# Kernel tuning notes

Hardware: AMD Instinct MI355X
Metric: run time of the kernel (lower is better)

Reference implementation:

```python
import jax, jax.numpy as jnp
import numpy as np

D = 1024           # fusion_dim
H_MHA = 16         # fusion_heads
H_GAT = 8          # graph attention heads
GAT_DH = D // H_GAT
DIL = (1, 2, 4, 8, 16)
K = 7              # temporal_kernel_size
B, T = 8, 256


def setup_inputs() -> dict:
    key = jax.random.key(0)
    ks = jax.random.split(key, 20)

    def w(k, sh, fan):
        return jax.random.normal(k, sh, jnp.float32) * np.float32(1.0 / np.sqrt(fan))

    inp = {"features": jax.random.normal(ks[0], (B, T, D), jnp.float32)}
    for i, dil in enumerate(DIL):
        inp["conv_w%d" % i] = w(ks[1 + i], (D, D, K), D * K)   # torch Conv1d (out, in, k)
        inp["conv_b%d" % i] = jnp.zeros((D,), jnp.float32)
    inp["fp_w"] = w(ks[6], (D, 5 * D), 5 * D)                    # torch Linear (out, in)
    inp["fp_b"] = jnp.zeros((D,), jnp.float32)
    inp["ln_g"] = jnp.ones((D,), jnp.float32)
    inp["ln_b"] = jnp.zeros((D,), jnp.float32)
    inp["wq"] = w(ks[7], (D, D), D); inp["bq"] = jnp.zeros((D,), jnp.float32)
    inp["wk"] = w(ks[8], (D, D), D); inp["bk"] = jnp.zeros((D,), jnp.float32)
    inp["wv"] = w(ks[9], (D, D), D); inp["bv"] = jnp.zeros((D,), jnp.float32)
    inp["wo"] = w(ks[10], (D, D), D); inp["bo"] = jnp.zeros((D,), jnp.float32)
    inp["gat_w"] = w(ks[11], (D, D), D)
    inp["gat_b"] = jnp.zeros((D,), jnp.float32)
    # original `a` is (2*head_dim, 1) shared across heads; split into a1 (source) / a2 (target)
    inp["gat_a1"] = w(ks[12], (GAT_DH,), 2 * GAT_DH)
    inp["gat_a2"] = w(ks[13], (GAT_DH,), 2 * GAT_DH)
    return inp


def _forward(features, conv_ws, conv_bs, fp_w, fp_b, ln_g, ln_b,
             wq, bq, wk, bk, wv, bv, wo, bo, gat_w, gat_b, gat_a1, gat_a2):
    Bb, Tt, Dm = features.shape
    x = jnp.transpose(features, (0, 2, 1))                       # (B, D, T)
    feats = []
    for wgt, bias, dil in zip(conv_ws, conv_bs, DIL):
        pad = (K - 1) * dil // 2                                 # 'same' padding
        y = jax.lax.conv_general_dilated(
            x, wgt, window_strides=(1,), padding=[(pad, pad)],
            rhs_dilation=(dil,), dimension_numbers=("NCH", "OIH", "NCH"))
        feats.append(jnp.transpose(y + bias[None, :, None], (0, 2, 1)))
    ms = jnp.concatenate(feats, axis=-1)                         # (B, T, 5D)
    z = ms @ fp_w.T + fp_b                                       # (B, T, D)
    mu = jnp.mean(z, -1, keepdims=True)
    var = jnp.var(z, -1, keepdims=True)
    z = (z - mu) * jax.lax.rsqrt(var + 1e-5) * ln_g + ln_b       # LayerNorm
    z = jax.nn.gelu(z, approximate=False)
    # --- multi-head self attention (batch_first, no dropout at eval) ---
    dh = Dm // H_MHA
    q = (z @ wq.T + bq).reshape(Bb, Tt, H_MHA, dh)
    k = (z @ wk.T + bk).reshape(Bb, Tt, H_MHA, dh)
    v = (z @ wv.T + bv).reshape(Bb, Tt, H_MHA, dh)
    scores = jnp.einsum("bqhd,bkhd->bhqk", q, k) * np.float32(1.0 / np.sqrt(dh))
    attn = jax.nn.softmax(scores, axis=-1)
    ctx = jnp.einsum("bhqk,bkhd->bqhd", attn, v).reshape(Bb, Tt, Dm)
    att_out = ctx @ wo.T + bo
    # --- all-pairs graph attention over N = B*T nodes (GAT-style, a shared across heads) ---
    n = Bb * Tt
    hg = (att_out.reshape(n, Dm) @ gat_w.T + gat_b).reshape(n, H_GAT, GAT_DH)
    e1 = jnp.einsum("nhd,d->nh", hg, gat_a1)                     # a1 . h_i
    e2 = jnp.einsum("nhd,d->nh", hg, gat_a2)                     # a2 . h_j
    e = jax.nn.leaky_relu(e1[:, None, :] + e2[None, :, :], 0.2)  # (N, N, H) via broadcast
    alpha = jax.nn.softmax(e, axis=1)                            # normalize over j
    hp = jnp.einsum("ijh,jhd->ihd", alpha, hg).reshape(n, Dm)
    g = jax.nn.elu(hp).reshape(Bb, Tt, Dm)
    return g + features


def reference(features, conv_w0, conv_w1, conv_w2, conv_w3, conv_w4,
              conv_b0, conv_b1, conv_b2, conv_b3, conv_b4,
              fp_w, fp_b, ln_g, ln_b,
              wq, bq, wk, bk, wv, bv, wo, bo,
              gat_w, gat_b, gat_a1, gat_a2):
    return _forward(features,
                    (conv_w0, conv_w1, conv_w2, conv_w3, conv_w4),
                    (conv_b0, conv_b1, conv_b2, conv_b3, conv_b4),
                    fp_w, fp_b, ln_g, ln_b,
                    wq, bq, wk, bk, wv, bv, wo, bo,
                    gat_w, gat_b, gat_a1, gat_a2)
```

## Files before the change

### kernel.cpp

```cpp
#include <hip/hip_runtime.h>
#include <hip/hip_bf16.h>

typedef __bf16 bf16_t;
typedef bf16_t bf16x8 __attribute__((ext_vector_type(8)));
typedef bf16_t bf16x4v __attribute__((ext_vector_type(4)));
typedef float f32x4 __attribute__((ext_vector_type(4)));

__device__ __forceinline__ void gll16(const bf16_t* g, bf16_t* l) {
    __builtin_amdgcn_global_load_lds(
        (const __attribute__((address_space(1))) unsigned int*)g,
        (__attribute__((address_space(3))) unsigned int*)l, 16, 0, 0);
}

__global__ __launch_bounds__(256)
void cvt_f32_bf16(const float* __restrict__ in, bf16_t* __restrict__ out, int n4)
{
    int i = blockIdx.x * 256 + threadIdx.x;
    if (i < n4) {
        float4 v = ((const float4*)in)[i];
        bf16x4v o = { (bf16_t)v.x, (bf16_t)v.y, (bf16_t)v.z, (bf16_t)v.w };
        *(bf16x4v*)&out[i * 4] = o;
    }
}

__global__ __launch_bounds__(256)
void cvt_multi(const float* __restrict__ fpw, const float* __restrict__ wq,
               const float* __restrict__ wk, const float* __restrict__ wv,
               const float* __restrict__ gw,
               bf16_t* __restrict__ fpwb, bf16_t* __restrict__ wqb,
               bf16_t* __restrict__ wkb, bf16_t* __restrict__ wvb,
               bf16_t* __restrict__ gwb)
{
    int id = blockIdx.x * 256 + threadIdx.x;
    const float* src; bf16_t* dst; int off;
    if (id < 1310720) { src = fpw; dst = fpwb; off = id; }
    else {
        int id3 = id - 1310720;
        int w = id3 >> 18; off = id3 & 262143;
        const float* ss[4] = {wq, wk, wv, gw};
        bf16_t* dd[4] = {wqb, wkb, wvb, gwb};
        src = ss[w]; dst = dd[w];
    }
    float4 v = ((const float4*)src)[off];
    bf16x4v o = { (bf16_t)v.x, (bf16_t)v.y, (bf16_t)v.z, (bf16_t)v.w };
    *(bf16x4v*)&dst[off * 4] = o;
}

__global__ __launch_bounds__(256)
void reorder_convw(const float* w0, const float* w1, const float* w2,
                   const float* w3, const float* w4, bf16_t* __restrict__ out)
{
    int gid = blockIdx.x * 256 + threadIdx.x;
    int i = gid >> 20, rem = gid & 1048575;
    int o = rem >> 10, c = rem & 1023;
    const float* ws[5] = {w0, w1, w2, w3, w4};
    const float* src = ws[i] + (size_t)o * 7168 + c * 7;
    #pragma unroll
    for (int kk = 0; kk < 7; kk++)
        out[((size_t)(i * 7 + kk) << 20) + (o << 10) + c] = (bf16_t)src[kk];
}

__global__ __launch_bounds__(256)
void gather_bias(const float* b0, const float* b1, const float* b2,
                 const float* b3, const float* b4,
                 const float* bq, const float* bk,
                 float* __restrict__ out, float* __restrict__ qkbias,
                 bf16_t* __restrict__ zp)
{
    int idx = blockIdx.x * 256 + threadIdx.x;
    if (blockIdx.x == 0 && threadIdx.x < 32) zp[threadIdx.x] = (bf16_t)0.0f;
    if (idx < 5120) {
        const float* bs[5] = {b0, b1, b2, b3, b4};
        out[idx] = bs[idx >> 10][idx & 1023];
    } else {
        int j = idx - 5120;
        qkbias[j] = (j < 1024) ? bq[j] : bk[j - 1024];
    }
}

__global__ __launch_bounds__(256)
void transpose_w(const float* __restrict__ in, bf16_t* __restrict__ out)
{
    __shared__ float tile[32][33];
    const int t = threadIdx.x;
    const int j0 = blockIdx.x * 32, c0 = blockIdx.y * 32;
    {
        int jl = t >> 3, cl = (t & 7) * 4;
        float4 v = *(const float4*)(in + (size_t)(j0 + jl) * 1024 + c0 + cl);
        tile[jl][cl] = v.x; tile[jl][cl + 1] = v.y;
        tile[jl][cl + 2] = v.z; tile[jl][cl + 3] = v.w;
    }
    __syncthreads();
    {
        int cl = t >> 3, jl = (t & 7) * 4;
        bf16x4v o = { (bf16_t)tile[jl][cl], (bf16_t)tile[jl + 1][cl],
                      (bf16_t)tile[jl + 2][cl], (bf16_t)tile[jl + 3][cl] };
        *(bf16x4v*)&out[(size_t)(c0 + cl) * 1024 + j0 + jl] = o;
    }
}

__global__ __launch_bounds__(256)
void fold_bias(const float* __restrict__ gw, const float* __restrict__ bo,
               const float* __restrict__ gb, float* __restrict__ bc)
{
    const int wave = threadIdx.x >> 6, lane = threadIdx.x & 63;
    const int d = blockIdx.x * 4 + wave;
    const float* row = gw + (size_t)d * 1024;
    float s = 0.f;
    #pragma unroll
    for (int k = lane * 4; k < 1024; k += 256) {
        float4 x = *(const float4*)&row[k];
        float4 a = *(const float4*)&bo[k];
        s += x.x * a.x + x.y * a.y + x.z * a.z + x.w * a.w;
    }
    s += __shfl_xor(s, 1);  s += __shfl_xor(s, 2);  s += __shfl_xor(s, 4);
    s += __shfl_xor(s, 8);  s += __shfl_xor(s, 16); s += __shfl_xor(s, 32);
    if (lane == 0) bc[d] = gb[d] + s;
}

template<bool CONV, bool OUT_BF16, bool BIAS_ROW = false, int NR = 128>
__global__ __launch_bounds__(256)
void mfma_gemm(const bf16_t* __restrict__ A, const bf16_t* __restrict__ Bw,
               const float* __restrict__ bias, void* __restrict__ outv,
               const bf16_t* __restrict__ zp,
               int Kd, int lda, int ldb, int ldo, int out_col0)
{
    constexpr int FN = NR / 32;
    __shared__ __align__(16) bf16_t As[3][NR * 32];
    __shared__ __align__(16) bf16_t Bs[3][128 * 32];
    const int t = threadIdx.x;
    const int lane = t & 63, wave = t >> 6;
    const int wn = (wave & 1) * (NR / 2), wm = (wave >> 1) * 64;
    const int q = lane >> 4, lr = lane & 15;
    const int mt = CONV ? (blockIdx.x & 7) : blockIdx.x;
    const int conv_i = CONV ? (blockIdx.x >> 3) : 0;
    const int m0 = mt * 128, n0 = blockIdx.y * NR;
    const int srow = lane >> 2, sseg = lane & 3;
    const int sw_seg = sseg ^ ((srow >> 1) & 3);
    const int slotq = (q ^ ((lr >> 1) & 3)) * 8;

    f32x4 acc[FN][4];
    #pragma unroll
    for (int a = 0; a < FN; a++)
        #pragma unroll
        for (int b = 0; b < 4; b++) acc[a][b] = (f32x4){0.f, 0.f, 0.f, 0.f};

    const int ksteps = Kd >> 5;
    const int T = CONV ? ksteps * 7 : ksteps;

    int s_tap = 0, s_k0 = 0;
    auto do_stage = [&](int bi) {
        const bf16_t* Bp = CONV ? (Bw + ((size_t)(conv_i * 7 + s_tap) << 20)) : Bw;
        const int shift = CONV ? ((s_tap - 3) << conv_i) : 0;
        #pragma unroll
        for (int p = 0; p < NR / 64; p++) {
            const int slab = p * 64 + wave * 16;
            const bf16_t* ga;
            if (CONV) {
                const int slabN = n0 + slab;
                const int inSeg = slabN & 255;
                if (inSeg + shift >= 0 && inSeg + shift <= 240) {
                    ga = A + (size_t)(slabN + srow + shift) * lda + s_k0 + sw_seg * 8;
                } else {
                    int n = slabN + srow;
                    int tg = (n & 255) + shift;
                    ga = ((unsigned)tg < 256u)
                       ? A + (size_t)((n & ~255) + tg) * lda + s_k0 + sw_seg * 8
                       : zp + sseg * 8;
                }
            } else {
                ga = A + (size_t)(n0 + slab + srow) * lda + s_k0 + sw_seg * 8;
            }
            gll16(ga, &As[bi][slab * 32]);
        }
        #pragma unroll
        for (int p = 0; p < 2; p++) {
            const int slab = p * 64 + wave * 16;
            const int rr = slab + srow;
            gll16(Bp + (size_t)(m0 + rr) * ldb + s_k0 + sw_seg * 8, &Bs[bi][slab * 32]);
        }
        s_k0 += 32;
        if (CONV && s_k0 == Kd) { s_k0 = 0; s_tap++; }
    };

    do_stage(0);
    do_stage(1);

    int cur = 0;
    for (int s = 0; s < T; s++) {
        if (s + 1 < T) {
            if constexpr (NR == 128) asm volatile("s_waitcnt vmcnt(4)" ::: "memory");
            else                     asm volatile("s_waitcnt vmcnt(3)" ::: "memory");
        } else {
            asm volatile("s_waitcnt vmcnt(0)" ::: "memory");
        }
        __builtin_amdgcn_s_barrier();
        __builtin_amdgcn_sched_barrier(0);

        bf16x8 af[FN], bfv[4];
        #pragma unroll
        for (int f = 0; f < FN; f++)
            af[f] = *(bf16x8*)&As[cur][(wn + f * 16 + lr) * 32 + slotq];
        #pragma unroll
        for (int f = 0; f < 4; f++)
            bfv[f] = *(bf16x8*)&Bs[cur][(wm + f * 16 + lr) * 32 + slotq];

        int nb = cur + 2; if (nb >= 3) nb -= 3;
        if (s + 2 < T) do_stage(nb);

        __builtin_amdgcn_s_setprio(1);
        #pragma unroll
        for (int fn = 0; fn < FN; fn++)
            #pragma unroll
            for (int fm = 0; fm < 4; fm++)
                acc[fn][fm] = __builtin_amdgcn_mfma_f32_16x16x32_bf16(
                    af[fn], bfv[fm], acc[fn][fm], 0, 0, 0);
        __builtin_amdgcn_s_setprio(0);
        cur++; if (cur == 3) cur = 0;
    }

    const int oc0 = CONV ? (conv_i << 10) : out_col0;
    #pragma unroll
    for (int fn = 0; fn < FN; fn++) {
        #pragma unroll
        for (int r = 0; r < 4; r++) {
            int n = n0 + wn + fn * 16 + q * 4 + r;
            #pragma unroll
            for (int fm = 0; fm < 4; fm++) {
                int m = m0 + wm + fm * 16 + lr;
                float v = acc[fn][fm][r];
                if (bias) v += bias[BIAS_ROW ? n : (oc0 + m)];
                if (OUT_BF16)
                    ((bf16_t*)outv)[(size_t)n * ldo + oc0 + m] = (bf16_t)v;
                else
                    ((float*)outv)[(size_t)n * ldo + oc0 + m] = v;
            }
        }
    }
}

__global__ __launch_bounds__(256)
void ln_gelu(float* __restrict__ z, bf16_t* __restrict__ zb,
             const float* __restrict__ g, const float* __restrict__ b)
{
    __shared__ float r1[256], r2[256];
    const int n = blockIdx.x, t = threadIdx.x;
    float* row = z + (size_t)n * 1024;
    float x[4], s = 0.f, s2 = 0.f;
    #pragma unroll
    for (int u = 0; u < 4; u++) {
        x[u] = row[t + u * 256];
        s += x[u]; s2 += x[u] * x[u];
    }
    r1[t] = s; r2[t] = s2;
    __syncthreads();
    for (int off = 128; off > 0; off >>= 1) {
        if (t < off) { r1[t] += r1[t + off]; r2[t] += r2[t + off]; }
        __syncthreads();
    }
    const float mu  = r1[0] * (1.0f / 1024.0f);
    const float var = r2[0] * (1.0f / 1024.0f) - mu * mu;
    const float rstd = rsqrtf(var + 1e-5f);
    #pragma unroll
    for (int u = 0; u < 4; u++) {
        int c = t + u * 256;
        float y = (x[u] - mu) * rstd * g[c] + b[c];
        float gv = 0.5f * y * (1.0f + erff(y * 0.70710678118654752f));
        row[c] = gv;
        zb[(size_t)n * 1024 + c] = (bf16_t)gv;
    }
}

__global__ __launch_bounds__(256)
void attn_mfma(const bf16_t* __restrict__ qg, const bf16_t* __restrict__ kg,
               const bf16_t* __restrict__ vt, bf16_t* __restrict__ ctx)
{
    const int it = blockIdx.x, h = blockIdx.y, bb = blockIdx.z;
    const int t = threadIdx.x, lane = t & 63, wave = t >> 6;
    const int q4 = lane >> 4, lr = lane & 15;
    const size_t qkbase = (size_t)bb * 256 * 2048 + (size_t)h * 64;

    __shared__ __align__(16) bf16_t Qs[4][32 * 64];
    __shared__ __align__(16) bf16_t Ks[64 * 64];
    __shared__ __align__(16) bf16_t Vs[64 * 64];
    __shared__ __align__(16) bf16_t Ps[4][32 * 64];

    {
        const int itbase = it * 128;
        #pragma unroll
        for (int rep = 0; rep < 4; rep++) {
            int idx = rep * 256 + t;
            int rl = idx >> 3, seg = idx & 7;
            bf16x8 v = *(const bf16x8*)&qg[qkbase + (size_t)(itbase + rl) * 2048 + seg * 8];
            *(bf16x8*)&Qs[rl >> 5][(rl & 31) * 64 + ((seg ^ (rl & 7)) << 3)] = v;
        }
    }

    f32x4 o[2][4];
    float mrow[2][4], lrow[2][4];
    #pragma unroll
    for (int fn = 0; fn < 2; fn++)
        #pragma unroll
        for (int x = 0; x < 4; x++) {
            o[fn][x] = (f32x4){0.f, 0.f, 0.f, 0.f};
            mrow[fn][x] = -1e30f; lrow[fn][x] = 0.f;
        }

    for (int j0 = 0; j0 < 256; j0 += 64) {
        __syncthreads();
        #pragma unroll
        for (int rep = 0; rep < 2; rep++) {
            int idx = rep * 256 + t;
            int rl = idx >> 3, seg = idx & 7;
            bf16x8 kv = *(const bf16x8*)&kg[qkbase + (size_t)(j0 + rl) * 2048 + seg * 8];
            *(bf16x8*)&Ks[rl * 64 + ((seg ^ (rl & 7)) << 3)] = kv;
            bf16x8 vv = *(const bf16x8*)&vt[(size_t)(h * 64 + rl) * 2048 + bb * 256 + j0 + seg * 8];
            *(bf16x8*)&Vs[rl * 64 + ((seg ^ (rl & 7)) << 3)] = vv;
        }
        __syncthreads();

        f32x4 s[2][4];
        #pragma unroll
        for (int fn = 0; fn < 2; fn++)
            #pragma unroll
            for (int fm = 0; fm < 4; fm++) s[fn][fm] = (f32x4){0.f, 0.f, 0.f, 0.f};
        #pragma unroll
        for (int kk = 0; kk < 2; kk++) {
            bf16x8 aq[2], bk[4];
            #pragma unroll
            for (int fn = 0; fn < 2; fn++) {
                int row = fn * 16 + lr;
                aq[fn] = *(bf16x8*)&Qs[wave][row * 64 + (((kk * 4 + q4) ^ (row & 7)) << 3)];
            }
            #pragma unroll
            for (int fm = 0; fm < 4; fm++) {
                int row = fm * 16 + lr;
                bk[fm] = *(bf16x8*)&Ks[row * 64 + (((kk * 4 + q4) ^ (row & 7)) << 3)];
            }
            #pragma unroll
            for (int fn = 0; fn < 2; fn++)
                #pragma unroll
                for (int fm = 0; fm < 4; fm++)
                    s[fn][fm] = __builtin_amdgcn_mfma_f32_16x16x32_bf16(
                        aq[fn], bk[fm], s[fn][fm], 0, 0, 0);
        }

        #pragma unroll
        for (int fn = 0; fn < 2; fn++) {
            #pragma unroll
            for (int r = 0; r < 4; r++) {
                float sv[4];
                #pragma unroll
                for (int fm = 0; fm < 4; fm++) sv[fm] = s[fn][fm][r] * 0.125f;
                float rm = fmaxf(fmaxf(sv[0], sv[1]), fmaxf(sv[2], sv[3]));
                rm = fmaxf(rm, __shfl_xor(rm, 1));
                rm = fmaxf(rm, __shfl_xor(rm, 2));
                rm = fmaxf(rm, __shfl_xor(rm, 4));
                rm = fmaxf(rm, __shfl_xor(rm, 8));
                float mold = mrow[fn][r];
                float mnew = fmaxf(mold, rm);
                float scl = __expf(mold - mnew);
                mrow[fn][r] = mnew;
                int prow = fn * 16 + q4 * 4 + r;
                float psum = 0.f;
                #pragma unroll
                for (int fm = 0; fm < 4; fm++) {
                    float p = __expf(sv[fm] - mnew);
                    psum += p;
                    int col = fm * 16 + lr;
                    Ps[wave][prow * 64 + (col ^ ((prow & 7) << 3))] = (bf16_t)p;
                }
                psum += __shfl_xor(psum, 1);
                psum += __shfl_xor(psum, 2);
                psum += __shfl_xor(psum, 4);
                psum += __shfl_xor(psum, 8);
                lrow[fn][r] = lrow[fn][r] * scl + psum;
                #pragma unroll
                for (int fd = 0; fd < 4; fd++) o[fn][fd][r] *= scl;
            }
        }

        #pragma unroll
        for (int kk = 0; kk < 2; kk++) {
            bf16x8 ap[2], bvf[4];
            #pragma unroll
            for (int fn = 0; fn < 2; fn++) {
                int row = fn * 16 + lr;
                ap[fn] = *(bf16x8*)&Ps[wave][row * 64 + (((kk * 4 + q4) ^ (row & 7)) << 3)];
            }
            #pragma unroll
            for (int fd = 0; fd < 4; fd++) {
                int row = fd * 16 + lr;
                bvf[fd] = *(bf16x8*)&Vs[row * 64 + (((kk * 4 + q4) ^ (row & 7)) << 3)];
            }
            #pragma unroll
            for (int fn = 0; fn < 2; fn++)
                #pragma unroll
                for (int fd = 0; fd < 4; fd++)
                    o[fn][fd] = __builtin_amdgcn_mfma_f32_16x16x32_bf16(
                        ap[fn], bvf[fd], o[fn][fd], 0, 0, 0);
        }
    }

    const int i0 = it * 128 + wave * 32;
    #pragma unroll
    for (int fn = 0; fn < 2; fn++) {
        #pragma unroll
        for (int r = 0; r < 4; r++) {
            float inv = 1.0f / lrow[fn][r];
            int row = i0 + fn * 16 + q4 * 4 + r;
            #pragma unroll
            for (int fd = 0; fd < 4; fd++) {
                int col = h * 64 + fd * 16 + lr;
                ctx[(size_t)bb * 262144 + (size_t)row * 1024 + col] =
                    (bf16_t)(o[fn][fd][r] * inv);
            }
        }
    }
}

__global__ __launch_bounds__(256)
void gat_e(const bf16_t* __restrict__ hgT, const float* __restrict__ a1,
           const float* __restrict__ a2, float* __restrict__ e1t,
           float* __restrict__ e2t)
{
    int id = blockIdx.x * 256 + threadIdx.x;
    int h = id >> 11, n = id & 2047;
    const bf16_t* base = hgT + (size_t)(h * 128) * 2048 + n;
    float s1 = 0.f, s2 = 0.f;
    #pragma unroll 4
    for (int d = 0; d < 128; d++) {
        float x = (float)base[(size_t)d * 2048];
        s1 += x * a1[d];
        s2 += x * a2[d];
    }
    e1t[id] = s1; e2t[id] = s2;
}

__global__ __launch_bounds__(256)
void gat_agg_mfma(const bf16_t* __restrict__ hgT, const float* __restrict__ e1t,
                  const float* __restrict__ e2t, const float* __restrict__ feat,
                  float* __restrict__ outp)
{
    const int it = blockIdx.x, h = blockIdx.y;
    const int i0 = it * 64;
    __shared__ float e2s[2048];
    __shared__ float e1s[64], mS[64], lSinv[64];
    __shared__ float wmax[4];
    __shared__ __align__(16) bf16_t Ps[64 * 136];
    __shared__ __align__(16) bf16_t Hs[128 * 136];
    const int t = threadIdx.x;
    const int lane = t & 63, wave = t >> 6;
    const int q = lane >> 4, lr = lane & 15;
    const int wm = wave * 32;

    float lmax = -1e30f;
    for (int idx = t; idx < 2048; idx += 256) {
        float v = e2t[h * 2048 + idx];
        e2s[idx] = v;
        lmax = fmaxf(lmax, v);
    }
    if (t < 64) e1s[t] = e1t[h * 2048 + i0 + t];
    #pragma unroll
    for (int d = 1; d < 64; d <<= 1) lmax = fmaxf(lmax, __shfl_xor(lmax, d));
    if (lane == 0) wmax[wave] = lmax;
    __syncthreads();
    {
        float maxE2 = fmaxf(fmaxf(wmax[0], wmax[1]), fmaxf(wmax[2], wmax[3]));
        if (t < 64) {
            float x = e1s[t] + maxE2;
            mS[t] = (x >= 0.f) ? x : 0.2f * x;
        }
    }
    __syncthreads();

    f32x4 acc[4][2];
    #pragma unroll
    for (int a = 0; a < 4; a++)
        #pragma unroll
        for (int b = 0; b < 2; b++) acc[a][b] = (f32x4){0.f, 0.f, 0.f, 0.f};
    float psum[4] = {0.f, 0.f, 0.f, 0.f};

    for (int j0 = 0; j0 < 2048; j0 += 128) {
        for (int idx = t; idx < 2048; idx += 256) {
            int d = idx >> 4, seg = idx & 15;
            *(bf16x8*)&Hs[d * 136 + seg * 8] =
                *(const bf16x8*)&hgT[(size_t)(h * 128 + d) * 2048 + j0 + seg * 8];
        }
        #pragma unroll
        for (int rep = 0; rep < 4; rep++) {
            int idx = rep * 256 + t;
            int i = idx >> 4, jg = idx & 15;
            float ei = e1s[i], mi = mS[i];
            bf16x8 pv;
            #pragma unroll
            for (int u = 0; u < 8; u++) {
                float x = ei + e2s[j0 + jg * 8 + u];
                x = (x >= 0.f) ? x : 0.2f * x;
                float p = __expf(x - mi);
                psum[rep] += p;
                pv[u] = (bf16_t)p;
            }
            *(bf16x8*)&Ps[i * 136 + jg * 8] = pv;
        }
        __syncthreads();
        #pragma unroll
        for (int kb = 0; kb < 4; kb++) {
            bf16x8 af[4], bf2[2];
            #pragma unroll
            for (int fn = 0; fn < 4; fn++)
                af[fn] = *(bf16x8*)&Ps[(fn * 16 + lr) * 136 + kb * 32 + q * 8];
            #pragma unroll
            for (int fm = 0; fm < 2; fm++)
                bf2[fm] = *(bf16x8*)&Hs[(wm + fm * 16 + lr) * 136 + kb * 32 + q * 8];
            #pragma unroll
            for (int fn = 0; fn < 4; fn++)
                #pragma unroll
                for (int fm = 0; fm < 2; fm++)
                    acc[fn][fm] = __builtin_amdgcn_mfma_f32_16x16x32_bf16(
                        af[fn], bf2[fm], acc[fn][fm], 0, 0, 0);
        }
        __syncthreads();
    }

    #pragma unroll
    for (int rep = 0; rep < 4; rep++) {
        float v = psum[rep];
        v += __shfl_xor(v, 1);
        v += __shfl_xor(v, 2);
        v += __shfl_xor(v, 4);
        v += __shfl_xor(v, 8);
        if ((t & 15) == 0) lSinv[rep * 16 + (t >> 4)] = 1.0f / v;
    }
    __syncthreads();

    #pragma unroll
    for (int fn = 0; fn < 4; fn++) {
        #pragma unroll
        for (int r = 0; r < 4; r++) {
            int il = fn * 16 + q * 4 + r;
            int i = i0 + il;
            float inv = lSinv[il];
            #pragma unroll
            for (int fm = 0; fm < 2; fm++) {
                int col = h * 128 + wm + fm * 16 + lr;
                float v = acc[fn][fm][r] * inv;
                v = (v > 0.f) ? v : (expf(v) - 1.0f);
                size_t off = (size_t)i * 1024 + col;
                outp[off] = v + feat[off];
            }
        }
    }
}

extern "C" void kernel_launch(void* const* d_in, const int* in_sizes, int n_in,
                              void* d_out, int out_size, void* d_ws, size_t ws_size,
                              hipStream_t stream)
{
    const float* feat = (const float*)d_in[0];
    const float *cw[5], *cb[5];
    if (in_sizes[2] == 1024) {
        for (int i = 0; i < 5; i++) { cw[i] = (const float*)d_in[1 + 2*i]; cb[i] = (const float*)d_in[2 + 2*i]; }
    } else {
        for (int i = 0; i < 5; i++) { cw[i] = (const float*)d_in[1 + i];   cb[i] = (const float*)d_in[6 + i]; }
    }
    const float* fp_w = (const float*)d_in[11];
    const float* fp_b = (const float*)d_in[12];
    const float* ln_g = (const float*)d_in[13];
    const float* ln_b = (const float*)d_in[14];
    const float* wq = (const float*)d_in[15]; const float* bq = (const float*)d_in[16];
    const float* wk = (const float*)d_in[17]; const float* bk = (const float*)d_in[18];
    const float* wv = (const float*)d_in[19]; const float* bv = (const float*)d_in[20];
    const float* wo = (const float*)d_in[21]; const float* bo = (const float*)d_in[22];
    const float* gat_w = (const float*)d_in[23]; const float* gat_b = (const float*)d_in[24];
    const float* ga1 = (const float*)d_in[25]; const float* ga2 = (const float*)d_in[26];
    float* outp = (float*)d_out;

    char* wsb = (char*)d_ws;
    bf16_t* xb    = (bf16_t*)(wsb);
    bf16_t* msb   = (bf16_t*)(wsb + 4194304);
    bf16_t* wcb   = (bf16_t*)(wsb + 25165824);
    float*  zf    = (float*) (wsb + 98566144);
    bf16_t* zb    = (bf16_t*)(wsb + 106954752);
    bf16_t* qb    = (bf16_t*)(wsb + 111149056);
    bf16_t* kb    = (bf16_t*)(wsb + 115343360);
    bf16_t* vb    = (bf16_t*)(wsb + 119537664);
    float*  cball = (float*) (wsb + 123731968);
    float*  e1t   = (float*) (wsb + 123752448);
    float*  e2t   = (float*) (wsb + 123817984);
    bf16_t* zpage = (bf16_t*)(wsb + 123883520);
    bf16_t* fpwb = wcb;
    bf16_t* wqb  = wcb + 5242880;
    bf16_t* wkb  = wqb + 1048576;
    bf16_t* wvb  = wkb + 1048576;
    bf16_t* woTb = wvb + 1048576;
    bf16_t* gwb  = woTb + 1048576;
    bf16_t* qkb  = qb;
    float*  qkbias = e1t;
    bf16_t* ctxb = zb;
    bf16_t* wcomb = xb;
    float*  bcomb = cball;
    bf16_t* hgtb = msb;

    const dim3 blk(256);

    cvt_f32_bf16<<<dim3(2048), blk, 0, stream>>>(feat, xb, 524288);
    reorder_convw<<<dim3(20480), blk, 0, stream>>>(cw[0], cw[1], cw[2], cw[3], cw[4], wcb);
    gather_bias<<<dim3(28), blk, 0, stream>>>(cb[0], cb[1], cb[2], cb[3], cb[4],
                                              bq, bk, cball, qkbias, zpage);

    mfma_gemm<true, true><<<dim3(40, 16), blk, 0, stream>>>(
        xb, wcb, cball, msb, zpage, 1024, 1024, 1024, 5120, 0);

    cvt_multi<<<dim3(9216), blk, 0, stream>>>(fp_w, wq, wk, wv, gat_w,
                                              fpwb, wqb, wkb, wvb, gwb);
    transpose_w<<<dim3(32, 32), blk, 0, stream>>>(wo, woTb);
    fold_bias<<<dim3(256), blk, 0, stream>>>(gat_w, bo, gat_b, bcomb);

    mfma_gemm<false, true, false, 64><<<dim3(8, 16), blk, 0, stream>>>(
        gwb, woTb, nullptr, wcomb, zpage, 1024, 1024, 1024, 1024, 0);

    mfma_gemm<false, false, false, 64><<<dim3(8, 32), blk, 0, stream>>>(
        msb, fpwb, fp_b, zf, zpage, 5120, 5120, 5120, 1024, 0);

    ln_gelu<<<dim3(2048), blk, 0, stream>>>(zf, zb, ln_g, ln_b);

    mfma_gemm<false, true, false, 64><<<dim3(16, 32), blk, 0, stream>>>(
        zb, wqb, qkbias, qkb, zpage, 1024, 1024, 1024, 2048, 0);
    mfma_gemm<false, true, true, 64><<<dim3(16, 16), blk, 0, stream>>>(
        wvb, zb, bv, vb, zpage, 1024, 1024, 1024, 2048, 0);

    attn_mfma<<<dim3(2, 16, 8), blk, 0, stream>>>(qkb, qkb + 1024, vb, ctxb);

    mfma_gemm<false, true, true, 64><<<dim3(16, 16), blk, 0, stream>>>(
        wcomb, ctxb, bcomb, hgtb, zpage, 1024, 1024, 1024, 2048, 0);

    gat_e<<<dim3(64), blk, 0, stream>>>(hgtb, ga1, ga2, e1t, e2t);
    gat_agg_mfma<<<dim3(32, 8), blk, 0, stream>>>(hgtb, e1t, e2t, feat, outp);
}
```

Measured before the change: 658.6 us.

## Merge prep kernels, batch independent GEMMs into dual launches, specialize conv GEMM

The small weight-conversion, bias-gather and transpose kernels are folded into two multi-role prep kernels. The conv weight reorder now stages each output row through shared memory so reads and writes are coalesced. Independent GEMMs (fp projection with the wo/gat weight fold, and QK with V) now share one grid split by blockIdx.y, which cuts launch count and fills more CUs. The conv GEMM becomes a dedicated kernel that precomputes per-tap pointers and steps them incrementally instead of recomputing addresses each k-step, at the cost of more code and extra register pressure.

Measured after the change: 641.1 us. -2.7%, faster.

```diff
diff --git a/kernel.cpp b/kernel.cpp
--- a/kernel.cpp
+++ b/kernel.cpp
@@ -13,128 +13,125 @@
 }
 
 __global__ __launch_bounds__(256)
-void cvt_f32_bf16(const float* __restrict__ in, bf16_t* __restrict__ out, int n4)
-{
-    int i = blockIdx.x * 256 + threadIdx.x;
-    if (i < n4) {
-        float4 v = ((const float4*)in)[i];
+void prep1(const float* w0, const float* w1, const float* w2, const float* w3,
+           const float* w4, const float* feat,
+           const float* b0, const float* b1, const float* b2, const float* b3,
+           const float* b4, const float* bq, const float* bk,
+           bf16_t* __restrict__ wout, bf16_t* __restrict__ xb,
+           float* __restrict__ cball, float* __restrict__ qkbias,
+           bf16_t* __restrict__ zp)
+{
+    __shared__ __align__(16) float s[7168];
+    const int bid = blockIdx.x, t = threadIdx.x;
+    if (bid < 5120) {
+        int i = bid >> 10, o = bid & 1023;
+        const float* ws[5] = {w0, w1, w2, w3, w4};
+        const float* src = ws[i] + (size_t)o * 7168;
+        #pragma unroll
+        for (int r = 0; r < 7; r++)
+            ((float4*)s)[r * 256 + t] = ((const float4*)src)[r * 256 + t];
+        __syncthreads();
+        const int c4 = t * 4;
+        #pragma unroll
+        for (int kk = 0; kk < 7; kk++) {
+            bf16x4v v = { (bf16_t)s[c4 * 7 + kk], (bf16_t)s[(c4 + 1) * 7 + kk],
+                          (bf16_t)s[(c4 + 2) * 7 + kk], (bf16_t)s[(c4 + 3) * 7 + kk] };
+            *(bf16x4v*)&wout[((size_t)(i * 7 + kk) << 20) + (o << 10) + c4] = v;
+        }
+    } else if (bid < 7168) {
+        int i = (bid - 5120) * 256 + t;
+        float4 v = ((const float4*)feat)[i];
+        bf16x4v o4 = { (bf16_t)v.x, (bf16_t)v.y, (bf16_t)v.z, (bf16_t)v.w };
+        *(bf16x4v*)&xb[i * 4] = o4;
+    } else {
+        int idx = (bid - 7168) * 256 + t;
+        if (bid == 7168 && t < 32) zp[t] = (bf16_t)0.0f;
+        if (idx < 5120) {
+            const float* bs[5] = {b0, b1, b2, b3, b4};
+            cball[idx] = bs[idx >> 10][idx & 1023];
+        } else {
+            int j = idx - 5120;
+            qkbias[j] = (j < 1024) ? bq[j] : bk[j - 1024];
+        }
+    }
+}
+
+__global__ __launch_bounds__(256)
+void prep2(const float* __restrict__ fpw, const float* __restrict__ wq,
+           const float* __restrict__ wk, const float* __restrict__ wv,
+           const float* __restrict__ gw, const float* __restrict__ wo,
+           const float* __restrict__ bo, const float* __restrict__ gb,
+           bf16_t* __restrict__ fpwb, bf16_t* __restrict__ wqb,
+           bf16_t* __restrict__ wkb, bf16_t* __restrict__ wvb,
+           bf16_t* __restrict__ gwb, bf16_t* __restrict__ woTb,
+           float* __restrict__ bc)
+{
+    __shared__ float tile[32][33];
+    const int bid = blockIdx.x, t = threadIdx.x;
+    if (bid < 9216) {
+        int id = bid * 256 + t;
+        const float* src; bf16_t* dst; int off;
+        if (id < 1310720) { src = fpw; dst = fpwb; off = id; }
+        else {
+            int id3 = id - 1310720;
+            int w = id3 >> 18; off = id3 & 262143;
+            const float* ss[4] = {wq, wk, wv, gw};
+            bf16_t* dd[4] = {wqb, wkb, wvb, gwb};
+            src = ss[w]; dst = dd[w];
+        }
+        float4 v = ((const float4*)src)[off];
         bf16x4v o = { (bf16_t)v.x, (bf16_t)v.y, (bf16_t)v.z, (bf16_t)v.w };
-        *(bf16x4v*)&out[i * 4] = o;
-    }
-}
-
-__global__ __launch_bounds__(256)
-void cvt_multi(const float* __restrict__ fpw, const float* __restrict__ wq,
-               const float* __restrict__ wk, const float* __restrict__ wv,
-               const float* __restrict__ gw,
-               bf16_t* __restrict__ fpwb, bf16_t* __restrict__ wqb,
-               bf16_t* __restrict__ wkb, bf16_t* __restrict__ wvb,
-               bf16_t* __restrict__ gwb)
-{
-    int id = blockIdx.x * 256 + threadIdx.x;
-    const float* src; bf16_t* dst; int off;
-    if (id < 1310720) { src = fpw; dst = fpwb; off = id; }
-    else {
-        int id3 = id - 1310720;
-        int w = id3 >> 18; off = id3 & 262143;
-        const float* ss[4] = {wq, wk, wv, gw};
-        bf16_t* dd[4] = {wqb, wkb, wvb, gwb};
-        src = ss[w]; dst = dd[w];
-    }
-    float4 v = ((const float4*)src)[off];
-    bf16x4v o = { (bf16_t)v.x, (bf16_t)v.y, (bf16_t)v.z, (bf16_t)v.w };
-    *(bf16x4v*)&dst[off * 4] = o;
-}
-
-__global__ __launch_bounds__(256)
-void reorder_convw(const float* w0, const float* w1, const float* w2,
-                   const float* w3, const float* w4, bf16_t* __restrict__ out)
-{
-    int gid = blockIdx.x * 256 + threadIdx.x;
-    int i = gid >> 20, rem = gid & 1048575;
-    int o = rem >> 10, c = rem & 1023;
-    const float* ws[5] = {w0, w1, w2, w3, w4};
-    const float* src = ws[i] + (size_t)o * 7168 + c * 7;
-    #pragma unroll
-    for (int kk = 0; kk < 7; kk++)
-        out[((size_t)(i * 7 + kk) << 20) + (o << 10) + c] = (bf16_t)src[kk];
-}
-
-__global__ __launch_bounds__(256)
-void gather_bias(const float* b0, const float* b1, const float* b2,
-                 const float* b3, const float* b4,
-                 const float* bq, const float* bk,
-                 float* __restrict__ out, float* __restrict__ qkbias,
-                 bf16_t* __restrict__ zp)
-{
-    int idx = blockIdx.x * 256 + threadIdx.x;
-    if (blockIdx.x == 0 && threadIdx.x < 32) zp[threadIdx.x] = (bf16_t)0.0f;
-    if (idx < 5120) {
-        const float* bs[5] = {b0, b1, b2, b3, b4};
-        out[idx] = bs[idx >> 10][idx & 1023];
+        *(bf16x4v*)&dst[off * 4] = o;
+    } else if (bid < 10240) {
+        int idx = bid - 9216;
+        int j0 = (idx & 31) * 32, c0 = (idx >> 5) * 32;
+        {
+            int jl = t >> 3, cl = (t & 7) * 4;
+            float4 v = *(const float4*)(wo + (size_t)(j0 + jl) * 1024 + c0 + cl);
+            tile[jl][cl] = v.x; tile[jl][cl + 1] = v.y;
+            tile[jl][cl + 2] = v.z; tile[jl][cl + 3] = v.w;
+        }
+        __syncthreads();
+        {
+            int cl = t >> 3, jl = (t & 7) * 4;
+            bf16x4v o = { (bf16_t)tile[jl][cl], (bf16_t)tile[jl + 1][cl],
+                          (bf16_t)tile[jl + 2][cl], (bf16_t)tile[jl + 3][cl] };
+            *(bf16x4v*)&woTb[(size_t)(c0 + cl) * 1024 + j0 + jl] = o;
+        }
     } else {
-        int j = idx - 5120;
-        qkbias[j] = (j < 1024) ? bq[j] : bk[j - 1024];
-    }
-}
-
-__global__ __launch_bounds__(256)
-void transpose_w(const float* __restrict__ in, bf16_t* __restrict__ out)
-{
-    __shared__ float tile[32][33];
-    const int t = threadIdx.x;
-    const int j0 = blockIdx.x * 32, c0 = blockIdx.y * 32;
-    {
-        int jl = t >> 3, cl = (t & 7) * 4;
-        float4 v = *(const float4*)(in + (size_t)(j0 + jl) * 1024 + c0 + cl);
-        tile[jl][cl] = v.x; tile[jl][cl + 1] = v.y;
-        tile[jl][cl + 2] = v.z; tile[jl][cl + 3] = v.w;
-    }
-    __syncthreads();
-    {
-        int cl = t >> 3, jl = (t & 7) * 4;
-        bf16x4v o = { (bf16_t)tile[jl][cl], (bf16_t)tile[jl + 1][cl],
-                      (bf16_t)tile[jl + 2][cl], (bf16_t)tile[jl + 3][cl] };
-        *(bf16x4v*)&out[(size_t)(c0 + cl) * 1024 + j0 + jl] = o;
-    }
-}
-
-__global__ __launch_bounds__(256)
-void fold_bias(const float* __restrict__ gw, const float* __restrict__ bo,
-               const float* __restrict__ gb, float* __restrict__ bc)
-{
-    const int wave = threadIdx.x >> 6, lane = threadIdx.x & 63;
-    const int d = blockIdx.x * 4 + wave;
-    const float* row = gw + (size_t)d * 1024;
-    float s = 0.f;
-    #pragma unroll
-    for (int k = lane * 4; k < 1024; k += 256) {
-        float4 x = *(const float4*)&row[k];
-        float4 a = *(const float4*)&bo[k];
-        s += x.x * a.x + x.y * a.y + x.z * a.z + x.w * a.w;
-    }
-    s += __shfl_xor(s, 1);  s += __shfl_xor(s, 2);  s += __shfl_xor(s, 4);
-    s += __shfl_xor(s, 8);  s += __shfl_xor(s, 16); s += __shfl_xor(s, 32);
-    if (lane == 0) bc[d] = gb[d] + s;
-}
-
-template<bool CONV, bool OUT_BF16, bool BIAS_ROW = false, int NR = 128>
-__global__ __launch_bounds__(256)
-void mfma_gemm(const bf16_t* __restrict__ A, const bf16_t* __restrict__ Bw,
-               const float* __restrict__ bias, void* __restrict__ outv,
-               const bf16_t* __restrict__ zp,
-               int Kd, int lda, int ldb, int ldo, int out_col0)
-{
-    constexpr int FN = NR / 32;
-    __shared__ __align__(16) bf16_t As[3][NR * 32];
-    __shared__ __align__(16) bf16_t Bs[3][128 * 32];
-    const int t = threadIdx.x;
-    const int lane = t & 63, wave = t >> 6;
+        int wave = t >> 6, lane = t & 63;
+        int d = (bid - 10240) * 4 + wave;
+        const float* row = gw + (size_t)d * 1024;
+        float ssum = 0.f;
+        #pragma unroll
+        for (int k = lane * 4; k < 1024; k += 256) {
+            float4 x = *(const float4*)&row[k];
+            float4 a = *(const float4*)&bo[k];
+            ssum += x.x * a.x + x.y * a.y + x.z * a.z + x.w * a.w;
+        }
+        ssum += __shfl_xor(ssum, 1);  ssum += __shfl_xor(ssum, 2);
+        ssum += __shfl_xor(ssum, 4);  ssum += __shfl_xor(ssum, 8);
+        ssum += __shfl_xor(ssum, 16); ssum += __shfl_xor(ssum, 32);
+        if (lane == 0) bc[d] = gb[d] + ssum;
+    }
+}
+
+struct GemmP {
+    const bf16_t* A; const bf16_t* Bw; const float* bias; void* outv;
+    int Kd, lda, ldb, ldo, flags;
+};
+
+template<int NR>
+__device__ __forceinline__ void gemm_body(char* smemraw, const GemmP P,
+                                          int bx, int by)
+{
+    constexpr int FN = NR / 32, NA = NR / 64;
+    auto As = (bf16_t(*)[NR * 32])smemraw;
+    auto Bs = (bf16_t(*)[128 * 32])(smemraw + 3 * NR * 32 * 2);
+    const int t = threadIdx.x, lane = t & 63, wave = t >> 6;
     const int wn = (wave & 1) * (NR / 2), wm = (wave >> 1) * 64;
     const int q = lane >> 4, lr = lane & 15;
-    const int mt = CONV ? (blockIdx.x & 7) : blockIdx.x;
-    const int conv_i = CONV ? (blockIdx.x >> 3) : 0;
-    const int m0 = mt * 128, n0 = blockIdx.y * NR;
+    const int m0 = bx * 128, n0 = by * NR;
     const int srow = lane >> 2, sseg = lane & 3;
     const int sw_seg = sseg ^ ((srow >> 1) & 3);
     const int slotq = (q ^ ((lr >> 1) & 3)) * 8;
@@ -145,44 +142,27 @@
         #pragma unroll
         for (int b = 0; b < 4; b++) acc[a][b] = (f32x4){0.f, 0.f, 0.f, 0.f};
 
-    const int ksteps = Kd >> 5;
-    const int T = CONV ? ksteps * 7 : ksteps;
-
-    int s_tap = 0, s_k0 = 0;
+    const bf16_t* aptr[NA]; const bf16_t* bptr[2];
+    #pragma unroll
+    for (int p = 0; p < NA; p++)
+        aptr[p] = P.A + (size_t)(n0 + p * 64 + wave * 16 + srow) * P.lda + sw_seg * 8;
+    #pragma unroll
+    for (int p = 0; p < 2; p++)
+        bptr[p] = P.Bw + (size_t)(m0 + p * 64 + wave * 16 + srow) * P.ldb + sw_seg * 8;
+
+    const int T = P.Kd >> 5;
     auto do_stage = [&](int bi) {
-        const bf16_t* Bp = CONV ? (Bw + ((size_t)(conv_i * 7 + s_tap) << 20)) : Bw;
-        const int shift = CONV ? ((s_tap - 3) << conv_i) : 0;
-        #pragma unroll
-        for (int p = 0; p < NR / 64; p++) {
-            const int slab = p * 64 + wave * 16;
-            const bf16_t* ga;
-            if (CONV) {
-                const int slabN = n0 + slab;
-                const int inSeg = slabN & 255;
-                if (inSeg + shift >= 0 && inSeg + shift <= 240) {
-                    ga = A + (size_t)(slabN + srow + shift) * lda + s_k0 + sw_seg * 8;
-                } else {
-                    int n = slabN + srow;
-                    int tg = (n & 255) + shift;
-                    ga = ((unsigned)tg < 256u)
-                       ? A + (size_t)((n & ~255) + tg) * lda + s_k0 + sw_seg * 8
-                       : zp + sseg * 8;
-                }
-            } else {
-                ga = A + (size_t)(n0 + slab + srow) * lda + s_k0 + sw_seg * 8;
-            }
-            gll16(ga, &As[bi][slab * 32]);
+        #pragma unroll
+        for (int p = 0; p < NA; p++) {
+            gll16(aptr[p], &As[bi][(p * 64 + wave * 16) * 32]);
+            aptr[p] += 32;
         }
         #pragma unroll
         for (int p = 0; p < 2; p++) {
-            const int slab = p * 64 + wave * 16;
-            const int rr = slab + srow;
-            gll16(Bp + (size_t)(m0 + rr) * ldb + s_k0 + sw_seg * 8, &Bs[bi][slab * 32]);
-        }
-        s_k0 += 32;
-        if (CONV && s_k0 == Kd) { s_k0 = 0; s_tap++; }
+            gll16(bptr[p], &Bs[bi][(p * 64 + wave * 16) * 32]);
+            bptr[p] += 32;
+        }
     };
-
     do_stage(0);
     do_stage(1);
 
@@ -219,7 +199,7 @@
         cur++; if (cur == 3) cur = 0;
     }
 
-    const int oc0 = CONV ? (conv_i << 10) : out_col0;
+    const bool obf = P.flags & 1, brow = P.flags & 2;
     #pragma unroll
     for (int fn = 0; fn < FN; fn++) {
         #pragma unroll
@@ -229,11 +209,140 @@
             for (int fm = 0; fm < 4; fm++) {
                 int m = m0 + wm + fm * 16 + lr;
                 float v = acc[fn][fm][r];
-                if (bias) v += bias[BIAS_ROW ? n : (oc0 + m)];
-                if (OUT_BF16)
-                    ((bf16_t*)outv)[(size_t)n * ldo + oc0 + m] = (bf16_t)v;
-                else
-                    ((float*)outv)[(size_t)n * ldo + oc0 + m] = v;
+                if (P.bias) v += P.bias[brow ? n : m];
+                if (obf) ((bf16_t*)P.outv)[(size_t)n * P.ldo + m] = (bf16_t)v;
+                else     ((float*)P.outv)[(size_t)n * P.ldo + m] = v;
+            }
+        }
+    }
+}
+
+template<int NR>
+__global__ __launch_bounds__(256)
+void mfma_gemm_one(GemmP P)
+{
+    __shared__ __align__(16) char smem[3 * NR * 32 * 2 + 3 * 128 * 32 * 2];
+    gemm_body<NR>(smem, P, blockIdx.x, blockIdx.y);
+}
+
+template<int NR>
+__global__ __launch_bounds__(256)
+void mfma_gemm_dual(GemmP P0, GemmP P1, int ysplit)
+{
+    __shared__ __align__(16) char smem[3 * NR * 32 * 2 + 3 * 128 * 32 * 2];
+    if ((int)blockIdx.y < ysplit)
+        gemm_body<NR>(smem, P0, blockIdx.x, blockIdx.y);
+    else
+        gemm_body<NR>(smem, P1, blockIdx.x, blockIdx.y - ysplit);
+}
+
+__global__ __launch_bounds__(256)
+void mfma_gemm_conv(const bf16_t* __restrict__ A, const bf16_t* __restrict__ Bw,
+                    const float* __restrict__ bias, bf16_t* __restrict__ out,
+                    const bf16_t* __restrict__ zp)
+{
+    __shared__ __align__(16) bf16_t As[3][128 * 32];
+    __shared__ __align__(16) bf16_t Bs[3][128 * 32];
+    const int t = threadIdx.x, lane = t & 63, wave = t >> 6;
+    const int wn = (wave & 1) * 64, wm = (wave >> 1) * 64;
+    const int q = lane >> 4, lr = lane & 15;
+    const int mt = blockIdx.x & 7, conv_i = blockIdx.x >> 3;
+    const int m0 = mt * 128, n0 = blockIdx.y * 128;
+    const int srow = lane >> 2, sseg = lane & 3;
+    const int sw_seg = sseg ^ ((srow >> 1) & 3);
+    const int slotq = (q ^ ((lr >> 1) & 3)) * 8;
+
+    f32x4 acc[4][4];
+    #pragma unroll
+    for (int a = 0; a < 4; a++)
+        #pragma unroll
+        for (int b = 0; b < 4; b++) acc[a][b] = (f32x4){0.f, 0.f, 0.f, 0.f};
+
+    const bf16_t* aptr[2]; int ainc[2];
+    const bf16_t* bptr[2];
+    int s_tap = 0, s_k0 = 0;
+
+    auto tap_init = [&]() {
+        const bf16_t* Bp = Bw + ((size_t)(conv_i * 7 + s_tap) << 20);
+        const int shift = (s_tap - 3) << conv_i;
+        #pragma unroll
+        for (int p = 0; p < 2; p++) {
+            const int slab = p * 64 + wave * 16;
+            const int slabN = n0 + slab;
+            const int inSeg = slabN & 255;
+            if (inSeg + shift >= 0 && inSeg + shift <= 240) {
+                aptr[p] = A + (size_t)(slabN + srow + shift) * 1024 + sw_seg * 8;
+                ainc[p] = 32;
+            } else {
+                int n = slabN + srow;
+                int tg = (n & 255) + shift;
+                bool ok = (unsigned)tg < 256u;
+                aptr[p] = ok ? A + (size_t)((n & ~255) + tg) * 1024 + sw_seg * 8
+                             : zp + sseg * 8;
+                ainc[p] = ok ? 32 : 0;
+            }
+            bptr[p] = Bp + (size_t)(m0 + slab + srow) * 1024 + sw_seg * 8;
+        }
+    };
+    auto do_stage = [&](int bi) {
+        #pragma unroll
+        for (int p = 0; p < 2; p++) {
+            const int slab = p * 64 + wave * 16;
+            gll16(aptr[p], &As[bi][slab * 32]);
+            gll16(bptr[p], &Bs[bi][slab * 32]);
+        }
+        s_k0 += 32;
+        if (s_k0 == 1024) {
+            s_k0 = 0; s_tap++;
+            if (s_tap < 7) tap_init();
+        } else {
+            #pragma unroll
+            for (int p = 0; p < 2; p++) { aptr[p] += ainc[p]; bptr[p] += 32; }
+        }
+    };
+
+    tap_init();
+    do_stage(0);
+    do_stage(1);
+
+    const int T = 224;
+    int cur = 0;
+    for (int s = 0; s < T; s++) {
+        if (s + 1 < T) asm volatile("s_waitcnt vmcnt(4)" ::: "memory");
+        else           asm volatile("s_waitcnt vmcnt(0)" ::: "memory");
+        __builtin_amdgcn_s_barrier();
+        __builtin_amdgcn_sched_barrier(0);
+
+        bf16x8 af[4], bfv[4];
+        #pragma unroll
+        for (int f = 0; f < 4; f++) {
+            af[f]  = *(bf16x8*)&As[cur][(wn + f * 16 + lr) * 32 + slotq];
+            bfv[f] = *(bf16x8*)&Bs[cur][(wm + f * 16 + lr) * 32 + slotq];
+        }
+        int nb = cur + 2; if (nb >= 3) nb -= 3;
+        if (s + 2 < T) do_stage(nb);
+
+        __builtin_amdgcn_s_setprio(1);
+        #pragma unroll
+        for (int fn = 0; fn < 4; fn++)
+            #pragma unroll
+            for (int fm = 0; fm < 4; fm++)
+                acc[fn][fm] = __builtin_amdgcn_mfma_f32_16x16x32_bf16(
+                    af[fn], bfv[fm], acc[fn][fm], 0, 0, 0);
+        __builtin_amdgcn_s_setprio(0);
+        cur++; if (cur == 3) cur = 0;
+    }
+
+    const int oc0 = conv_i << 10;
+    #pragma unroll
+    for (int fn = 0; fn < 4; fn++) {
+        #pragma unroll
+        for (int r = 0; r < 4; r++) {
+            int n = n0 + wn + fn * 16 + q * 4 + r;
+            #pragma unroll
+            for (int fm = 0; fm < 4; fm++) {
+                int m = m0 + wm + fm * 16 + lr;
+                out[(size_t)n * 5120 + oc0 + m] = (bf16_t)(acc[fn][fm][r] + bias[oc0 + m]);
             }
         }
     }
@@ -604,36 +713,35 @@
 
     const dim3 blk(256);
 
-    cvt_f32_bf16<<<dim3(2048), blk, 0, stream>>>(feat, xb, 524288);
-    reorder_convw<<<dim3(20480), blk, 0, stream>>>(cw[0], cw[1], cw[2], cw[3], cw[4], wcb);
-    gather_bias<<<dim3(28), blk, 0, stream>>>(cb[0], cb[1], cb[2], cb[3], cb[4],
-                                              bq, bk, cball, qkbias, zpage);
-
-    mfma_gemm<true, true><<<dim3(40, 16), blk, 0, stream>>>(
-        xb, wcb, cball, msb, zpage, 1024, 1024, 1024, 5120, 0);
-
-    cvt_multi<<<dim3(9216), blk, 0, stream>>>(fp_w, wq, wk, wv, gat_w,
-                                              fpwb, wqb, wkb, wvb, gwb);
-    transpose_w<<<dim3(32, 32), blk, 0, stream>>>(wo, woTb);
-    fold_bias<<<dim3(256), blk, 0, stream>>>(gat_w, bo, gat_b, bcomb);
-
-    mfma_gemm<false, true, false, 64><<<dim3(8, 16), blk, 0, stream>>>(
-        gwb, woTb, nullptr, wcomb, zpage, 1024, 1024, 1024, 1024, 0);
-
-    mfma_gemm<false, false, false, 64><<<dim3(8, 32), blk, 0, stream>>>(
-        msb, fpwb, fp_b, zf, zpage, 5120, 5120, 5120, 1024, 0);
+    prep1<<<dim3(7196), blk, 0, stream>>>(cw[0], cw[1], cw[2], cw[3], cw[4], feat,
+                                          cb[0], cb[1], cb[2], cb[3], cb[4], bq, bk,
+                                          wcb, xb, cball, qkbias, zpage);
+
+    mfma_gemm_conv<<<dim3(40, 16), blk, 0, stream>>>(xb, wcb, cball, msb, zpage);
+
+    prep2<<<dim3(10496), blk, 0, stream>>>(fp_w, wq, wk, wv, gat_w, wo, bo, gat_b,
+                                           fpwb, wqb, wkb, wvb, gwb, woTb, bcomb);
+
+    {
+        GemmP pf  = { msb, fpwb, fp_b, zf,    5120, 5120, 5120, 1024, 0 };
+        GemmP pwc = { gwb, woTb, nullptr, wcomb, 1024, 1024, 1024, 1024, 1 };
+        mfma_gemm_dual<64><<<dim3(8, 48), blk, 0, stream>>>(pf, pwc, 32);
+    }
 
     ln_gelu<<<dim3(2048), blk, 0, stream>>>(zf, zb, ln_g, ln_b);
 
-    mfma_gemm<false, true, false, 64><<<dim3(16, 32), blk, 0, stream>>>(
-        zb, wqb, qkbias, qkb, zpage, 1024, 1024, 1024, 2048, 0);
-    mfma_gemm<false, true, true, 64><<<dim3(16, 16), blk, 0, stream>>>(
-        wvb, zb, bv, vb, zpage, 1024, 1024, 1024, 2048, 0);
+    {
+        GemmP pqk = { zb,  wqb, qkbias, qkb, 1024, 1024, 1024, 2048, 1 };
+        GemmP pv  = { wvb, zb,  bv,     vb,  1024, 1024, 1024, 2048, 3 };
+        mfma_gemm_dual<64><<<dim3(16, 48), blk, 0, stream>>>(pqk, pv, 32);
+    }
 
     attn_mfma<<<dim3(2, 16, 8), blk, 0, stream>>>(qkb, qkb + 1024, vb, ctxb);
 
-    mfma_gemm<false, true, true, 64><<<dim3(16, 16), blk, 0, stream>>>(
-        wcomb, ctxb, bcomb, hgtb, zpage, 1024, 1024, 1024, 2048, 0);
+    {
+        GemmP pg = { wcomb, ctxb, bcomb, hgtb, 1024, 1024, 1024, 2048, 3 };
+        mfma_gemm_one<64><<<dim3(16, 16), blk, 0, stream>>>(pg);
+    }
 
     gat_e<<<dim3(64), blk, 0, stream>>>(hgtb, ga1, ga2, e1t, e2t);
     gat_agg_mfma<<<dim3(32, 8), blk, 0, stream>>>(hgtb, e1t, e2t, feat, outp);
```
